# Kernel tuning notes

Measured on AMD Instinct MI355X. Metric: run time of the kernel, lower is better.

Reference implementation:

```python
import jax, jax.numpy as jnp
import numpy as np

B, S, D = 2048, 8, 1280
K = 1                 # n_components_remove
HIGH_T = 0.6          # PC1_HIGH_ACTIVITY_THRESHOLD
STORM_T = 0.8         # solar_storm_threshold


def setup_inputs() -> dict:
    key = jax.random.key(0)
    k1, k2 = jax.random.split(key, 2)
    features = jax.random.normal(k1, (B, S, D), dtype=jnp.float32)
    kp_index = jax.random.uniform(k2, (B,), dtype=jnp.float32) * 9.0
    cmr_gate = jnp.ones((1,), dtype=jnp.float32)  # nn.Parameter(torch.ones(1))
    return {"features": features, "kp_index": kp_index, "cmr_gate": cmr_gate}


def reference(features, kp_index, cmr_gate):
    # Per-sample standardization over the feature axis (numpy std, ddof=0)
    mu = features.mean(axis=2, keepdims=True)            # (B, S, 1)
    sigma = features.std(axis=2, keepdims=True) + 1e-8   # (B, S, 1)
    fn = (features - mu) / sigma                         # (B, S, D)

    # Batched thin SVD of the (S, D) normalized feature matrix
    U, sv, Vt = jnp.linalg.svd(fn, full_matrices=False)  # (B,S,S), (B,S), (B,S,D)
    var = sv * sv
    pc1_ratio = var[:, 0] / (var.sum(axis=-1) + 1e-8)    # (B,)

    # solar_flag: 0 normal, 1 high activity, 2 storm
    solar_flag = (pc1_ratio >= HIGH_T).astype(jnp.int32) + (pc1_ratio >= STORM_T).astype(jnp.int32)

    # Rank-K reconstruction of the common-mode (solar) component
    low = jnp.einsum('bsk,bk,bkd->bsd', U[:, :, :K], sv[:, :K], Vt[:, :K, :])
    clean = (fn - low) * sigma + mu                      # de-normalized cleaned features

    # Kp-gating: amplify CMR when Kp >= 5
    kp_gate = 1.0 + 0.5 * (kp_index >= 5.0).astype(features.dtype)[:, None, None]
    clean = features + kp_gate * (clean - features)

    # Learnable gate
    gate = jax.nn.sigmoid(cmr_gate)[0]
    features_clean = features + gate * (clean - features)
    return features_clean, pc1_ratio, solar_flag
```

## Files before the change

### kernel.cpp

```cpp
#include <hip/hip_runtime.h>
#include <math.h>


#define SV 8
#define DV 1280
#define D4 320
#define BSTRIDE (SV*DV)
#define GSZ 136
#define SPLIT 4
#define CITER (40/SPLIT)

typedef __attribute__((ext_vector_type(8))) short bf16x8;
typedef __attribute__((ext_vector_type(4))) float f32x4;

union BF8 { bf16x8 v; short s[8]; unsigned u[4]; };

__global__ __launch_bounds__(256, 2)
void cmr_fused(const float* __restrict__ feat,
               const float* __restrict__ kp,
               const float* __restrict__ cmr_gate,
               float* __restrict__ out, int Bn)
{
    __shared__ float lg[SPLIT][2][GSZ];
    __shared__ float lc[2][17];

    const int tid  = threadIdx.x;
    const int lane = tid & 63;
    const int h    = tid >> 6;
    const int pair = blockIdx.x;

    {
        const int m    = lane & 15;
        const int quad = lane >> 4;
        const int bt   = m >> 3;
        const int row  = m & 7;

        const float* __restrict__ fb =
            feat + ((size_t)(pair * 2 + bt)) * BSTRIDE + (size_t)row * DV;

        BF8 ones;
#pragma unroll
        for (int j = 0; j < 4; ++j) ones.u[j] = 0x3F803F80u;

        f32x4 accHH = {0.f, 0.f, 0.f, 0.f};
        f32x4 accHL = {0.f, 0.f, 0.f, 0.f};
        f32x4 accS  = {0.f, 0.f, 0.f, 0.f};

#pragma unroll
        for (int c = 0; c < CITER; ++c) {
            const int k0 = (h * CITER + c) * 32 + quad * 8;
            const float4 x0 = *(const float4*)(fb + k0);
            const float4 x1 = *(const float4*)(fb + k0 + 4);
            float x[8] = {x0.x, x0.y, x0.z, x0.w, x1.x, x1.y, x1.z, x1.w};
            BF8 hi, lo;
#pragma unroll
            for (int j = 0; j < 4; ++j) {
                unsigned hp, lp;
                asm("v_cvt_pk_bf16_f32 %0, %1, %2"
                    : "=v"(hp) : "v"(x[2*j]), "v"(x[2*j+1]));
                const float h0 = __uint_as_float(hp << 16);
                const float h1 = __uint_as_float(hp & 0xFFFF0000u);
                const float l0 = x[2*j]     - h0;
                const float l1 = x[2*j + 1] - h1;
                asm("v_cvt_pk_bf16_f32 %0, %1, %2"
                    : "=v"(lp) : "v"(l0), "v"(l1));
                hi.u[j] = hp;
                lo.u[j] = lp;
            }
            accHH = __builtin_amdgcn_mfma_f32_16x16x32_bf16(hi.v, hi.v,   accHH, 0, 0, 0);
            accHL = __builtin_amdgcn_mfma_f32_16x16x32_bf16(hi.v, lo.v,   accHL, 0, 0, 0);
            accS  = __builtin_amdgcn_mfma_f32_16x16x32_bf16(hi.v, ones.v, accS,  0, 0, 0);
            accS  = __builtin_amdgcn_mfma_f32_16x16x32_bf16(lo.v, ones.v, accS,  0, 0, 0);
        }

        const int colb = (lane & 15) >> 3;
        const int col  = lane & 7;
#pragma unroll
        for (int r = 0; r < 4; ++r) {
            const int rowg = quad * 4 + r;
            if ((rowg >> 3) == colb) {
                lg[h][colb][(rowg & 7) * 8 + col]      = accHH[r];
                lg[h][colb][64 + (rowg & 7) * 8 + col] = accHL[r];
            }
        }
        if ((lane & 15) == 0) {
#pragma unroll
            for (int r = 0; r < 4; ++r) {
                const int rowg = quad * 4 + r;
                lg[h][rowg >> 3][128 + (rowg & 7)] = accS[r];
            }
        }
    }
    __syncthreads();

    if (h == 0 && lane < 2) {
        const int b2 = lane;
        const int b  = pair * 2 + b2;

        float G[8][8], S[8], mu[8], sig[8], rsig[8];
#pragma unroll
        for (int i = 0; i < 8; ++i) {
#pragma unroll
            for (int j = 0; j < 8; ++j) G[i][j] = 0.f;
            S[i] = 0.f;
        }
#pragma unroll
        for (int hh = 0; hh < SPLIT; ++hh) {
            const float* __restrict__ gh = &lg[hh][b2][0];
#pragma unroll
            for (int i = 0; i < 8; ++i) {
#pragma unroll
                for (int j = 0; j < 8; ++j)
                    G[i][j] += gh[i * 8 + j] + gh[64 + i * 8 + j] + gh[64 + j * 8 + i];
                S[i] += gh[128 + i];
            }
        }
        const float invD = 1.f / (float)DV;
#pragma unroll
        for (int i = 0; i < 8; ++i) {
            mu[i] = S[i] * invD;
            const float var = fmaxf(G[i][i] * invD - mu[i] * mu[i], 0.f);
            sig[i]  = sqrtf(var) + 1e-8f;
            rsig[i] = 1.f / sig[i];
        }
#pragma unroll
        for (int i = 0; i < 8; ++i)
#pragma unroll
            for (int j = 0; j < 8; ++j)
                G[i][j] = (G[i][j] - (float)DV * mu[i] * mu[j]) * rsig[i] * rsig[j];

        float tr = 0.f;
#pragma unroll
        for (int i = 0; i < 8; ++i) tr += G[i][i];

        float A[8][8];
        {
            const float rt = 1.f / fmaxf(tr, 1e-30f);
#pragma unroll
            for (int i = 0; i < 8; ++i)
#pragma unroll
                for (int j = 0; j < 8; ++j) A[i][j] = G[i][j] * rt;
        }
#pragma unroll
        for (int t = 0; t < 12; ++t) {
            float Bm[8][8];
            float trB = 0.f;
#pragma unroll
            for (int i = 0; i < 8; ++i)
#pragma unroll
                for (int j = i; j < 8; ++j) {
                    float acc = 0.f;
#pragma unroll
                    for (int k = 0; k < 8; ++k)
                        acc = fmaf(A[i][k], A[j][k], acc);
                    Bm[i][j] = acc;
                    if (i == j) trB += acc;
                }
            const float rt = 1.f / fmaxf(trB, 1e-30f);
#pragma unroll
            for (int i = 0; i < 8; ++i)
#pragma unroll
                for (int j = i; j < 8; ++j) {
                    const float v = Bm[i][j] * rt;
                    A[i][j] = v; A[j][i] = v;
                }
        }
        int bj = 0; float best = A[0][0];
#pragma unroll
        for (int k = 1; k < 8; ++k)
            if (A[k][k] > best) { best = A[k][k]; bj = k; }
        float u[8];
#pragma unroll
        for (int i = 0; i < 8; ++i) {
            float v = A[i][0];
#pragma unroll
            for (int k = 1; k < 8; ++k) v = (bj == k) ? A[i][k] : v;
            u[i] = v;
        }
        {
            float nn = 0.f;
#pragma unroll
            for (int i = 0; i < 8; ++i) nn = fmaf(u[i], u[i], nn);
            const float r = rsqrtf(fmaxf(nn, 1e-30f));
#pragma unroll
            for (int i = 0; i < 8; ++i) u[i] *= r;
        }
#pragma unroll
        for (int it = 0; it < 2; ++it) {
            float y[8]; float ny = 0.f;
#pragma unroll
            for (int i = 0; i < 8; ++i) {
                float acc = 0.f;
#pragma unroll
                for (int k = 0; k < 8; ++k) acc = fmaf(G[i][k], u[k], acc);
                y[i] = acc; ny = fmaf(acc, acc, ny);
            }
            const float r = rsqrtf(fmaxf(ny, 1e-30f));
#pragma unroll
            for (int i = 0; i < 8; ++i) u[i] = y[i] * r;
        }
        float lam = 0.f;
#pragma unroll
        for (int i = 0; i < 8; ++i) {
            float acc = 0.f;
#pragma unroll
            for (int k = 0; k < 8; ++k) acc = fmaf(G[i][k], u[k], acc);
            lam = fmaf(u[i], acc, lam);
        }
        const float pc1 = lam / (tr + 1e-8f);

        const float gate = 1.f / (1.f + expf(-cmr_gate[0]));
        const float kpg  = (kp[b] >= 5.0f) ? 1.5f : 1.0f;
        const float Gt   = gate * kpg;

        float bc = 0.f;
#pragma unroll
        for (int i = 0; i < 8; ++i) bc = fmaf(u[i] * rsig[i], mu[i], bc);

#pragma unroll
        for (int i = 0; i < 8; ++i) {
            lc[b2][i]     = u[i] * rsig[i];
            lc[b2][8 + i] = Gt * sig[i] * u[i];
        }
        lc[b2][16] = bc;
        out[(size_t)Bn * BSTRIDE + b] = pc1;
        out[(size_t)Bn * BSTRIDE + Bn + b] =
            (pc1 >= 0.6f ? 1.f : 0.f) + (pc1 >= 0.8f ? 1.f : 0.f);
    }
    __syncthreads();

    for (int u = tid; u < 2 * D4; u += 256) {
        const int b2  = (u >= D4) ? 1 : 0;
        const int col = u - b2 * D4;

        float a[8], c[8];
#pragma unroll
        for (int s = 0; s < 8; ++s) { a[s] = lc[b2][s]; c[s] = lc[b2][8 + s]; }
        const float bc = lc[b2][16];

        const float4* __restrict__ f4 =
            (const float4*)(feat + (size_t)(pair * 2 + b2) * BSTRIDE);
        float4* __restrict__ o4 =
            (float4*)(out + (size_t)(pair * 2 + b2) * BSTRIDE);

        float4 f[8];
#pragma unroll
        for (int s = 0; s < 8; ++s) f[s] = f4[s * D4 + col];

        float4 p = make_float4(-bc, -bc, -bc, -bc);
#pragma unroll
        for (int s = 0; s < 8; ++s) {
            p.x = fmaf(a[s], f[s].x, p.x);
            p.y = fmaf(a[s], f[s].y, p.y);
            p.z = fmaf(a[s], f[s].z, p.z);
            p.w = fmaf(a[s], f[s].w, p.w);
        }
#pragma unroll
        for (int s = 0; s < 8; ++s) {
            float4 o;
            o.x = fmaf(-c[s], p.x, f[s].x);
            o.y = fmaf(-c[s], p.y, f[s].y);
            o.z = fmaf(-c[s], p.z, f[s].z);
            o.w = fmaf(-c[s], p.w, f[s].w);
            o4[s * D4 + col] = o;
        }
    }
}

extern "C" void kernel_launch(void* const* d_in, const int* in_sizes, int n_in,
                              void* d_out, int out_size, void* d_ws, size_t ws_size,
                              hipStream_t stream) {
    const float* feat = (const float*)d_in[0];
    const float* kp   = (const float*)d_in[1];
    const float* gate = (const float*)d_in[2];
    float* out = (float*)d_out;
    const int Bn = in_sizes[0] / BSTRIDE;
    (void)d_ws; (void)ws_size;

    cmr_fused<<<Bn / 2, 256, 0, stream>>>(feat, kp, gate, out, Bn);
}
```

Measured before the change: 178.0 us.

## Stage sample features in LDS via global_load_lds, one sample per block

Each block now handles one sample instead of two, and loads its full 8x1280 feature tile into LDS with asynchronous global_load_lds before the Gram MFMA pass. The cleanup pass reads features from LDS rather than re-reading global memory, removing the second global read of the input. The Gram partial reduction is parallelised across a wavefront before a single lane runs the eigen solve. The cost is about 41KB of LDS per block, which limits occupancy, plus an extra barrier after staging and a serial solve that now runs once per sample per block.

New measurement: 189.2 us. +6.3%, slower.

```diff
diff --git a/kernel.cpp b/kernel.cpp
--- a/kernel.cpp
+++ b/kernel.cpp
@@ -6,14 +6,20 @@
 #define DV 1280
 #define D4 320
 #define BSTRIDE (SV*DV)
+#define LROW 1284
 #define GSZ 136
-#define SPLIT 4
-#define CITER (40/SPLIT)
+#define NSLOT 8
 
 typedef __attribute__((ext_vector_type(8))) short bf16x8;
 typedef __attribute__((ext_vector_type(4))) float f32x4;
 
 union BF8 { bf16x8 v; short s[8]; unsigned u[4]; };
+
+__device__ __forceinline__ void stage16(const float* g, float* l) {
+    __builtin_amdgcn_global_load_lds(
+        (const __attribute__((address_space(1))) unsigned*)g,
+        (__attribute__((address_space(3))) unsigned*)l, 16, 0, 0);
+}
 
 __global__ __launch_bounds__(256, 2)
 void cmr_fused(const float* __restrict__ feat,
@@ -21,22 +27,35 @@
                const float* __restrict__ cmr_gate,
                float* __restrict__ out, int Bn)
 {
-    __shared__ float lg[SPLIT][2][GSZ];
-    __shared__ float lc[2][17];
+    __shared__ float fl[SV * LROW];
+    __shared__ float lg[NSLOT][GSZ];
+    __shared__ float lc[17];
 
     const int tid  = threadIdx.x;
     const int lane = tid & 63;
     const int h    = tid >> 6;
-    const int pair = blockIdx.x;
+    const int b    = blockIdx.x;
 
     {
-        const int m    = lane & 15;
-        const int quad = lane >> 4;
-        const int bt   = m >> 3;
-        const int row  = m & 7;
-
-        const float* __restrict__ fb =
-            feat + ((size_t)(pair * 2 + bt)) * BSTRIDE + (size_t)row * DV;
+        const float* __restrict__ gb = feat + (size_t)b * BSTRIDE;
+#pragma unroll
+        for (int i = 0; i < 10; ++i) {
+            const int chunk = h * 10 + i;
+            const int r  = chunk / 5;
+            const int cc = chunk % 5;
+            stage16(gb + (size_t)r * DV + cc * 256 + lane * 4,
+                    &fl[r * LROW + cc * 256]);
+        }
+    }
+    __syncthreads();
+
+    {
+        const int m      = lane & 15;
+        const int quad   = lane >> 4;
+        const int row    = m & 7;
+        const int stream = h * 2 + (m >> 3);
+
+        const float* __restrict__ fr = &fl[row * LROW];
 
         BF8 ones;
 #pragma unroll
@@ -47,10 +66,10 @@
         f32x4 accS  = {0.f, 0.f, 0.f, 0.f};
 
 #pragma unroll
-        for (int c = 0; c < CITER; ++c) {
-            const int k0 = (h * CITER + c) * 32 + quad * 8;
-            const float4 x0 = *(const float4*)(fb + k0);
-            const float4 x1 = *(const float4*)(fb + k0 + 4);
+        for (int c = 0; c < 5; ++c) {
+            const int k0 = (stream * 5 + c) * 32 + quad * 8;
+            const float4 x0 = *(const float4*)(fr + k0);
+            const float4 x1 = *(const float4*)(fr + k0 + 4);
             float x[8] = {x0.x, x0.y, x0.z, x0.w, x1.x, x1.y, x1.z, x1.w};
             BF8 hi, lo;
 #pragma unroll
@@ -73,196 +92,192 @@
             accS  = __builtin_amdgcn_mfma_f32_16x16x32_bf16(lo.v, ones.v, accS,  0, 0, 0);
         }
 
-        const int colb = (lane & 15) >> 3;
+        const int colh = (lane & 15) >> 3;
         const int col  = lane & 7;
 #pragma unroll
         for (int r = 0; r < 4; ++r) {
             const int rowg = quad * 4 + r;
-            if ((rowg >> 3) == colb) {
-                lg[h][colb][(rowg & 7) * 8 + col]      = accHH[r];
-                lg[h][colb][64 + (rowg & 7) * 8 + col] = accHL[r];
+            if ((rowg >> 3) == colh) {
+                float* gs = &lg[h * 2 + colh][0];
+                gs[(rowg & 7) * 8 + col]      = accHH[r];
+                gs[64 + (rowg & 7) * 8 + col] = accHL[r];
             }
         }
         if ((lane & 15) == 0) {
 #pragma unroll
             for (int r = 0; r < 4; ++r) {
                 const int rowg = quad * 4 + r;
-                lg[h][rowg >> 3][128 + (rowg & 7)] = accS[r];
+                lg[h * 2 + (rowg >> 3)][128 + (rowg & 7)] = accS[r];
             }
         }
     }
     __syncthreads();
 
-    if (h == 0 && lane < 2) {
-        const int b2 = lane;
-        const int b  = pair * 2 + b2;
-
-        float G[8][8], S[8], mu[8], sig[8], rsig[8];
-#pragma unroll
-        for (int i = 0; i < 8; ++i) {
-#pragma unroll
-            for (int j = 0; j < 8; ++j) G[i][j] = 0.f;
-            S[i] = 0.f;
-        }
-#pragma unroll
-        for (int hh = 0; hh < SPLIT; ++hh) {
-            const float* __restrict__ gh = &lg[hh][b2][0];
+    if (h == 0) {
+        for (int idx = lane; idx < GSZ; idx += 64) {
+            float s = lg[0][idx];
+#pragma unroll
+            for (int hh = 1; hh < NSLOT; ++hh) s += lg[hh][idx];
+            lg[0][idx] = s;
+        }
+        asm volatile("s_waitcnt lgkmcnt(0)" ::: "memory");
+
+        if (lane == 0) {
+            const float* __restrict__ gh = &lg[0][0];
+            float G[8][8], S[8], mu[8], sig[8], rsig[8];
 #pragma unroll
             for (int i = 0; i < 8; ++i) {
 #pragma unroll
                 for (int j = 0; j < 8; ++j)
-                    G[i][j] += gh[i * 8 + j] + gh[64 + i * 8 + j] + gh[64 + j * 8 + i];
-                S[i] += gh[128 + i];
-            }
-        }
-        const float invD = 1.f / (float)DV;
-#pragma unroll
-        for (int i = 0; i < 8; ++i) {
-            mu[i] = S[i] * invD;
-            const float var = fmaxf(G[i][i] * invD - mu[i] * mu[i], 0.f);
-            sig[i]  = sqrtf(var) + 1e-8f;
-            rsig[i] = 1.f / sig[i];
-        }
-#pragma unroll
-        for (int i = 0; i < 8; ++i)
-#pragma unroll
-            for (int j = 0; j < 8; ++j)
-                G[i][j] = (G[i][j] - (float)DV * mu[i] * mu[j]) * rsig[i] * rsig[j];
-
-        float tr = 0.f;
-#pragma unroll
-        for (int i = 0; i < 8; ++i) tr += G[i][i];
-
-        float A[8][8];
-        {
-            const float rt = 1.f / fmaxf(tr, 1e-30f);
+                    G[i][j] = gh[i * 8 + j] + gh[64 + i * 8 + j] + gh[64 + j * 8 + i];
+                S[i] = gh[128 + i];
+            }
+            const float invD = 1.f / (float)DV;
+#pragma unroll
+            for (int i = 0; i < 8; ++i) {
+                mu[i] = S[i] * invD;
+                const float var = fmaxf(G[i][i] * invD - mu[i] * mu[i], 0.f);
+                sig[i]  = sqrtf(var) + 1e-8f;
+                rsig[i] = 1.f / sig[i];
+            }
 #pragma unroll
             for (int i = 0; i < 8; ++i)
 #pragma unroll
-                for (int j = 0; j < 8; ++j) A[i][j] = G[i][j] * rt;
-        }
-#pragma unroll
-        for (int t = 0; t < 12; ++t) {
-            float Bm[8][8];
-            float trB = 0.f;
-#pragma unroll
-            for (int i = 0; i < 8; ++i)
-#pragma unroll
-                for (int j = i; j < 8; ++j) {
+                for (int j = 0; j < 8; ++j)
+                    G[i][j] = (G[i][j] - (float)DV * mu[i] * mu[j]) * rsig[i] * rsig[j];
+
+            float tr = 0.f;
+#pragma unroll
+            for (int i = 0; i < 8; ++i) tr += G[i][i];
+
+            float A[8][8];
+            {
+                const float rt = 1.f / fmaxf(tr, 1e-30f);
+#pragma unroll
+                for (int i = 0; i < 8; ++i)
+#pragma unroll
+                    for (int j = 0; j < 8; ++j) A[i][j] = G[i][j] * rt;
+            }
+#pragma unroll
+            for (int t = 0; t < 12; ++t) {
+                float Bm[8][8];
+                float trB = 0.f;
+#pragma unroll
+                for (int i = 0; i < 8; ++i)
+#pragma unroll
+                    for (int j = i; j < 8; ++j) {
+                        float acc = 0.f;
+#pragma unroll
+                        for (int k = 0; k < 8; ++k)
+                            acc = fmaf(A[i][k], A[j][k], acc);
+                        Bm[i][j] = acc;
+                        if (i == j) trB += acc;
+                    }
+                const float rt = 1.f / fmaxf(trB, 1e-30f);
+#pragma unroll
+                for (int i = 0; i < 8; ++i)
+#pragma unroll
+                    for (int j = i; j < 8; ++j) {
+                        const float v = Bm[i][j] * rt;
+                        A[i][j] = v; A[j][i] = v;
+                    }
+            }
+            int bj = 0; float best = A[0][0];
+#pragma unroll
+            for (int k = 1; k < 8; ++k)
+                if (A[k][k] > best) { best = A[k][k]; bj = k; }
+            float u[8];
+#pragma unroll
+            for (int i = 0; i < 8; ++i) {
+                float v = A[i][0];
+#pragma unroll
+                for (int k = 1; k < 8; ++k) v = (bj == k) ? A[i][k] : v;
+                u[i] = v;
+            }
+            {
+                float nn = 0.f;
+#pragma unroll
+                for (int i = 0; i < 8; ++i) nn = fmaf(u[i], u[i], nn);
+                const float r = rsqrtf(fmaxf(nn, 1e-30f));
+#pragma unroll
+                for (int i = 0; i < 8; ++i) u[i] *= r;
+            }
+#pragma unroll
+            for (int it = 0; it < 2; ++it) {
+                float y[8]; float ny = 0.f;
+#pragma unroll
+                for (int i = 0; i < 8; ++i) {
                     float acc = 0.f;
 #pragma unroll
-                    for (int k = 0; k < 8; ++k)
-                        acc = fmaf(A[i][k], A[j][k], acc);
-                    Bm[i][j] = acc;
-                    if (i == j) trB += acc;
+                    for (int k = 0; k < 8; ++k) acc = fmaf(G[i][k], u[k], acc);
+                    y[i] = acc; ny = fmaf(acc, acc, ny);
                 }
-            const float rt = 1.f / fmaxf(trB, 1e-30f);
-#pragma unroll
-            for (int i = 0; i < 8; ++i)
-#pragma unroll
-                for (int j = i; j < 8; ++j) {
-                    const float v = Bm[i][j] * rt;
-                    A[i][j] = v; A[j][i] = v;
-                }
-        }
-        int bj = 0; float best = A[0][0];
-#pragma unroll
-        for (int k = 1; k < 8; ++k)
-            if (A[k][k] > best) { best = A[k][k]; bj = k; }
-        float u[8];
-#pragma unroll
-        for (int i = 0; i < 8; ++i) {
-            float v = A[i][0];
-#pragma unroll
-            for (int k = 1; k < 8; ++k) v = (bj == k) ? A[i][k] : v;
-            u[i] = v;
-        }
-        {
-            float nn = 0.f;
-#pragma unroll
-            for (int i = 0; i < 8; ++i) nn = fmaf(u[i], u[i], nn);
-            const float r = rsqrtf(fmaxf(nn, 1e-30f));
-#pragma unroll
-            for (int i = 0; i < 8; ++i) u[i] *= r;
-        }
-#pragma unroll
-        for (int it = 0; it < 2; ++it) {
-            float y[8]; float ny = 0.f;
+                const float r = rsqrtf(fmaxf(ny, 1e-30f));
+#pragma unroll
+                for (int i = 0; i < 8; ++i) u[i] = y[i] * r;
+            }
+            float lam = 0.f;
 #pragma unroll
             for (int i = 0; i < 8; ++i) {
                 float acc = 0.f;
 #pragma unroll
                 for (int k = 0; k < 8; ++k) acc = fmaf(G[i][k], u[k], acc);
-                y[i] = acc; ny = fmaf(acc, acc, ny);
-            }
-            const float r = rsqrtf(fmaxf(ny, 1e-30f));
-#pragma unroll
-            for (int i = 0; i < 8; ++i) u[i] = y[i] * r;
-        }
-        float lam = 0.f;
-#pragma unroll
-        for (int i = 0; i < 8; ++i) {
-            float acc = 0.f;
-#pragma unroll
-            for (int k = 0; k < 8; ++k) acc = fmaf(G[i][k], u[k], acc);
-            lam = fmaf(u[i], acc, lam);
-        }
-        const float pc1 = lam / (tr + 1e-8f);
-
-        const float gate = 1.f / (1.f + expf(-cmr_gate[0]));
-        const float kpg  = (kp[b] >= 5.0f) ? 1.5f : 1.0f;
-        const float Gt   = gate * kpg;
-
-        float bc = 0.f;
-#pragma unroll
-        for (int i = 0; i < 8; ++i) bc = fmaf(u[i] * rsig[i], mu[i], bc);
-
-#pragma unroll
-        for (int i = 0; i < 8; ++i) {
-            lc[b2][i]     = u[i] * rsig[i];
-            lc[b2][8 + i] = Gt * sig[i] * u[i];
-        }
-        lc[b2][16] = bc;
-        out[(size_t)Bn * BSTRIDE + b] = pc1;
-        out[(size_t)Bn * BSTRIDE + Bn + b] =
-            (pc1 >= 0.6f ? 1.f : 0.f) + (pc1 >= 0.8f ? 1.f : 0.f);
+                lam = fmaf(u[i], acc, lam);
+            }
+            const float pc1 = lam / (tr + 1e-8f);
+
+            const float gate = 1.f / (1.f + expf(-cmr_gate[0]));
+            const float kpg  = (kp[b] >= 5.0f) ? 1.5f : 1.0f;
+            const float Gt   = gate * kpg;
+
+            float bc = 0.f;
+#pragma unroll
+            for (int i = 0; i < 8; ++i) bc = fmaf(u[i] * rsig[i], mu[i], bc);
+
+#pragma unroll
+            for (int i = 0; i < 8; ++i) {
+                lc[i]     = u[i] * rsig[i];
+                lc[8 + i] = Gt * sig[i] * u[i];
+            }
+            lc[16] = bc;
+            out[(size_t)Bn * BSTRIDE + b] = pc1;
+            out[(size_t)Bn * BSTRIDE + Bn + b] =
+                (pc1 >= 0.6f ? 1.f : 0.f) + (pc1 >= 0.8f ? 1.f : 0.f);
+        }
     }
     __syncthreads();
 
-    for (int u = tid; u < 2 * D4; u += 256) {
-        const int b2  = (u >= D4) ? 1 : 0;
-        const int col = u - b2 * D4;
-
+    {
         float a[8], c[8];
 #pragma unroll
-        for (int s = 0; s < 8; ++s) { a[s] = lc[b2][s]; c[s] = lc[b2][8 + s]; }
-        const float bc = lc[b2][16];
-
-        const float4* __restrict__ f4 =
-            (const float4*)(feat + (size_t)(pair * 2 + b2) * BSTRIDE);
-        float4* __restrict__ o4 =
-            (float4*)(out + (size_t)(pair * 2 + b2) * BSTRIDE);
-
-        float4 f[8];
-#pragma unroll
-        for (int s = 0; s < 8; ++s) f[s] = f4[s * D4 + col];
-
-        float4 p = make_float4(-bc, -bc, -bc, -bc);
-#pragma unroll
-        for (int s = 0; s < 8; ++s) {
-            p.x = fmaf(a[s], f[s].x, p.x);
-            p.y = fmaf(a[s], f[s].y, p.y);
-            p.z = fmaf(a[s], f[s].z, p.z);
-            p.w = fmaf(a[s], f[s].w, p.w);
-        }
-#pragma unroll
-        for (int s = 0; s < 8; ++s) {
-            float4 o;
-            o.x = fmaf(-c[s], p.x, f[s].x);
-            o.y = fmaf(-c[s], p.y, f[s].y);
-            o.z = fmaf(-c[s], p.z, f[s].z);
-            o.w = fmaf(-c[s], p.w, f[s].w);
-            o4[s * D4 + col] = o;
+        for (int s = 0; s < 8; ++s) { a[s] = lc[s]; c[s] = lc[8 + s]; }
+        const float bc = lc[16];
+
+        float4* __restrict__ o4 = (float4*)(out + (size_t)b * BSTRIDE);
+
+        for (int col = tid; col < D4; col += 256) {
+            float4 f[8];
+#pragma unroll
+            for (int s = 0; s < 8; ++s)
+                f[s] = *(const float4*)&fl[s * LROW + col * 4];
+
+            float4 p = make_float4(-bc, -bc, -bc, -bc);
+#pragma unroll
+            for (int s = 0; s < 8; ++s) {
+                p.x = fmaf(a[s], f[s].x, p.x);
+                p.y = fmaf(a[s], f[s].y, p.y);
+                p.z = fmaf(a[s], f[s].z, p.z);
+                p.w = fmaf(a[s], f[s].w, p.w);
+            }
+#pragma unroll
+            for (int s = 0; s < 8; ++s) {
+                float4 o;
+                o.x = fmaf(-c[s], p.x, f[s].x);
+                o.y = fmaf(-c[s], p.y, f[s].y);
+                o.z = fmaf(-c[s], p.z, f[s].z);
+                o.w = fmaf(-c[s], p.w, f[s].w);
+                o4[s * D4 + col] = o;
+            }
         }
     }
 }
@@ -277,5 +292,5 @@
     const int Bn = in_sizes[0] / BSTRIDE;
     (void)d_ws; (void)ws_size;
 
-    cmr_fused<<<Bn / 2, 256, 0, stream>>>(feat, kp, gate, out, Bn);
+    cmr_fused<<<Bn, 256, 0, stream>>>(feat, kp, gate, out, Bn);
 }
```
